# Performance work log

Measured on AMD Instinct MI355X. Metric: run time of the kernel, lower is better.

## Reference

```python
import jax, jax.numpy as jnp
import numpy as np

B, FIN, V, X, Y, Z = 2, 32, 768, 8, 8, 8
K, FOUT = 5, 32
NNZ = V * 8  # ~8 neighbors per vertex


def setup_inputs() -> dict:
    key = jax.random.key(0)
    k1, k2, k3, k4, k5 = jax.random.split(key, 5)
    std = np.sqrt(2.0 / (FIN * K)).astype(np.float32)
    return {
        "lap_rows": jax.random.randint(k1, (NNZ,), 0, V, dtype=jnp.int32),
        "lap_cols": jax.random.randint(k2, (NNZ,), 0, V, dtype=jnp.int32),
        "lap_vals": jax.random.normal(k3, (NNZ,), dtype=jnp.float32) * 0.1,
        "x": jax.random.normal(k4, (B, FIN, V, X, Y, Z), dtype=jnp.float32),
        "weight": jax.random.normal(k5, (K, FIN, FOUT), dtype=jnp.float32) * std,
        "bias": jnp.full((FOUT,), 0.01, dtype=jnp.float32),
    }


def reference(lap_rows, lap_cols, lap_vals, x, weight, bias):
    Bb, Fin, Vv, Xx, Yy, Zz = x.shape
    Kk, _, Fout = weight.shape

    def spmm(v):  # sparse [V,V] @ dense [V,D]
        return jax.ops.segment_sum(lap_vals[:, None] * v[lap_cols],
                                   lap_rows, num_segments=Vv)

    # [B,Fin,V,X,Y,Z] -> [V, Fin*B*X*Y*Z]
    x0 = jnp.transpose(x, (2, 1, 0, 3, 4, 5)).reshape(Vv, -1)
    xs = [x0]
    if Kk > 1:
        x1 = spmm(x0)
        xs.append(x1)
        for _ in range(2, Kk):
            x2 = 2.0 * spmm(x1) - x0
            xs.append(x2)
            x0, x1 = x1, x2
    basis = jnp.stack(xs, axis=0)  # [K, V, Fin*B*X*Y*Z]
    basis = basis.reshape(Kk, Vv, Fin, Bb, Xx, Yy, Zz)
    basis = jnp.transpose(basis, (3, 1, 4, 5, 6, 0, 2))  # [B,V,X,Y,Z,K,Fin]
    out = basis.reshape(-1, Kk * Fin) @ weight.reshape(Kk * Fin, Fout)
    out = out.reshape(Bb, Vv, Xx, Yy, Zz, Fout)
    out = jnp.transpose(out, (0, 5, 1, 2, 3, 4))  # [B,Fout,V,X,Y,Z]
    return out + bias[None, :, None, None, None, None]
```

## Files before the change

### kernel.cpp

```cpp
#include <hip/hip_runtime.h>
#include <stdint.h>

#define V      768
#define FINC   32
#define FOUTC  32
#define XYZ    512
#define NB     2
#define ROWP   40
#define MAXDEG 32
#define EROWS  (MAXDEG + 2)

typedef unsigned short u16;
typedef unsigned int   u32;
typedef short bf16x8 __attribute__((ext_vector_type(8)));
typedef float f32x4  __attribute__((ext_vector_type(4)));
typedef float f32x2  __attribute__((ext_vector_type(2)));

__device__ __forceinline__ u16 f2bf(float f) {
  u32 u = __float_as_uint(f);
  u32 r = u + 0x7fffu + ((u >> 16) & 1u);
  return (u16)(r >> 16);
}
__device__ __forceinline__ float bflo(u32 w) { return __uint_as_float(w << 16); }
__device__ __forceinline__ float bfhi(u32 w) { return __uint_as_float(w & 0xffff0000u); }
__device__ __forceinline__ float bfhi_raw(u32 w) { return __uint_as_float(w); }
__device__ __forceinline__ u32 cvtpk_bf16(float lo, float hi) {
  u32 r;
  asm("v_cvt_pk_bf16_f32 %0, %1, %2" : "=v"(r) : "v"(lo), "v"(hi));
  return r;
}

__global__ __launch_bounds__(64) void build_ell(const int* __restrict__ rows,
                                                const int* __restrict__ cols,
                                                const float* __restrict__ vals,
                                                int nnz,
                                                int2* __restrict__ epair,
                                                int* __restrict__ deg) {
  int v = blockIdx.x;
  int lane = threadIdx.x;
  int cnt = 0;
  for (int base = 0; base < nnz; base += 64) {
    int i = base + lane;
    bool m = (i < nnz) && (rows[i] == v);
    unsigned long long mask = __ballot(m);
    if (m) {
      int pos = cnt + __popcll(mask & ((1ull << lane) - 1ull));
      if (pos < MAXDEG)
        epair[v * MAXDEG + pos] = make_int2(cols[i], __float_as_int(vals[i]));
    }
    cnt += __popcll(mask);
  }
  int d = cnt < MAXDEG ? cnt : MAXDEG;
  for (int p = d + lane; p < MAXDEG; p += 64)
    epair[v * MAXDEG + p] = make_int2(0, 0);
  if (lane == 0) deg[v] = d;
}

__global__ __launch_bounds__(V) void sort_rows(const int2* __restrict__ epair,
                                               const int* __restrict__ deg,
                                               int2* __restrict__ ep3,
                                               int* __restrict__ perm,
                                               int* __restrict__ inv_g,
                                               int* __restrict__ wtrip) {
  __shared__ int sdeg[V];
  __shared__ u16 sinv[V];
  int v = threadIdx.x;
  int d = deg[v];
  sdeg[v] = d;
  __syncthreads();
  int r = 0;
  for (int u = 0; u < V; ++u) {
    int du = sdeg[u];
    r += (du > d) || (du == d && u < v);
  }
  const unsigned long long GPK = 0x8495A6B73210ull;
  int w = (int)((GPK >> (4 * (r >> 6))) & 15ull);
  int p = w * 64 + (r & 63);
  perm[p] = v;
  inv_g[v] = p;
  sinv[v] = (u16)p;
  if ((r & 63) == 0) wtrip[w] = d;
  __syncthreads();
  for (int e = 0; e < EROWS; ++e) {
    int2 o = make_int2(0, 0);
    if (e < d) {
      int2 pe = epair[v * MAXDEG + e];
      o = make_int2((int)sinv[pe.x] * (ROWP * 2), pe.y);
    }
    ep3[e * V + p] = o;
  }
}

__global__ __launch_bounds__(512) void transpose_x(const float* __restrict__ x,
                                                   const int* __restrict__ inv_g,
                                                   u16* __restrict__ xT) {
  int g = blockIdx.x;
  int b = g / V, v = g - b * V;
  int pv = inv_g[v];
  int t = threadIdx.x;
  float vals[FINC];
  const float* src = x + ((size_t)(b * FINC) * V + v) * XYZ + t;
#pragma unroll
  for (int f = 0; f < FINC; ++f) vals[f] = src[(size_t)f * V * XYZ];
  u32 pw[16];
#pragma unroll
  for (int p = 0; p < 16; ++p)
    pw[p] = (u32)f2bf(vals[2 * p]) | ((u32)f2bf(vals[2 * p + 1]) << 16);
  uint4* dst = (uint4*)(xT + ((size_t)(b * XYZ + t) * V + pv) * FINC);
#pragma unroll
  for (int q = 0; q < 4; ++q)
    dst[q] = make_uint4(pw[4 * q], pw[4 * q + 1], pw[4 * q + 2], pw[4 * q + 3]);
}

__global__ __launch_bounds__(1024, 4) void cheb_main(
    const u16* __restrict__ xT, const int2* __restrict__ ep3,
    const int* __restrict__ perm, const int* __restrict__ wtrip,
    const float* __restrict__ weight, const float* __restrict__ bias,
    u32* __restrict__ stage) {
  __shared__ __align__(16) u16   CUR[V * ROWP];
  __shared__ __align__(16) uint4 WF[5][2][64];
  __shared__ u16 PRM[V];
  __shared__ int WT[12];

  int g = blockIdx.x;
  int xcd = g & 7;
  int u = g >> 3;
  int phase = u >> 5;
  int xyz = xcd * 32 + (u & 31) + (phase & 1) * 256;
  int b = phase >> 1;
  int slice = b * XYZ + xyz;

  int tid = threadIdx.x;
  int lane = tid & 63;
  int w = tid >> 6;
  int l15 = lane & 15, l4 = lane >> 4;
  bool gath = tid < V;

  if (tid < 640) {
    int k = tid >> 7, n = (tid >> 6) & 1, ln = tid & 63;
    int a15 = ln & 15, a4 = ln >> 4;
    u32 pw[4];
#pragma unroll
    for (int p = 0; p < 4; ++p) {
      float w0 = weight[(size_t)(k * FINC + a4 * 8 + 2 * p) * FOUTC + n * 16 + a15];
      float w1 = weight[(size_t)(k * FINC + a4 * 8 + 2 * p + 1) * FOUTC + n * 16 + a15];
      pw[p] = (u32)f2bf(w0) | ((u32)f2bf(w1) << 16);
    }
    WF[k][n][ln] = make_uint4(pw[0], pw[1], pw[2], pw[3]);
  }
  if (tid < 12) WT[tid] = wtrip[tid];
  if (gath) PRM[tid] = (u16)perm[tid];
  float bsv[2] = {bias[l15], bias[16 + l15]};

  u32 curpk[16], prevpk[16];
  if (gath) {
    const uint4* src = (const uint4*)(xT + (size_t)slice * V * FINC) + tid * 4;
    uint4* dst = (uint4*)(CUR + tid * ROWP);
#pragma unroll
    for (int j = 0; j < 4; ++j) {
      uint4 q = src[j];
      dst[j] = q;
      curpk[4 * j] = q.x; curpk[4 * j + 1] = q.y;
      curpk[4 * j + 2] = q.z; curpk[4 * j + 3] = q.w;
    }
  }
  __syncthreads();

  int trip = 0;
  if (w < 12) trip = __builtin_amdgcn_readfirstlane(WT[w]);
  const int2* pp = ep3 + tid;

  f32x4 acc[3][2];
#pragma unroll
  for (int a = 0; a < 3; ++a)
#pragma unroll
    for (int n = 0; n < 2; ++n) acc[a][n] = (f32x4){0.f, 0.f, 0.f, 0.f};

  auto gemm_acc = [&](int k) {
    bf16x8 bn0 = *(const bf16x8*)&WF[k][0][lane];
    bf16x8 bn1 = *(const bf16x8*)&WF[k][1][lane];
#pragma unroll
    for (int a = 0; a < 3; ++a) {
      int row = w * 48 + a * 16 + l15;
      bf16x8 af = *(const bf16x8*)(CUR + row * ROWP + l4 * 8);
      acc[a][0] = __builtin_amdgcn_mfma_f32_16x16x32_bf16(af, bn0, acc[a][0], 0, 0, 0);
      acc[a][1] = __builtin_amdgcn_mfma_f32_16x16x32_bf16(af, bn1, acc[a][1], 0, 0, 0);
    }
  };

  f32x2 fa2[16];
  auto gather = [&]() {
#pragma unroll
    for (int j = 0; j < 16; ++j) fa2[j] = (f32x2){0.f, 0.f};
    int2 pe0 = pp[0];
    int2 pe1 = pp[V];
    for (int e = 0; e < trip; ++e) {
      int2 nx = pp[(e + 2) * V];
      float fv = __int_as_float(pe0.y);
      f32x2 fv2 = {fv, fv};
      const uint4* sp = (const uint4*)((const char*)CUR + (u32)pe0.x);
      uint4 qa = sp[0], qb = sp[1], qc = sp[2], qd = sp[3];
      u32 wq[16] = {qa.x, qa.y, qa.z, qa.w, qb.x, qb.y, qb.z, qb.w,
                    qc.x, qc.y, qc.z, qc.w, qd.x, qd.y, qd.z, qd.w};
#pragma unroll
      for (int p = 0; p < 16; ++p) {
        f32x2 s = {bflo(wq[p]), bfhi_raw(wq[p])};
        fa2[p] += fv2 * s;
      }
      pe0 = pe1; pe1 = nx;
    }
  };

  auto store_cur = [&]() {
    uint4* dp = (uint4*)(CUR + tid * ROWP);
#pragma unroll
    for (int j = 0; j < 4; ++j)
      dp[j] = make_uint4(curpk[4 * j], curpk[4 * j + 1], curpk[4 * j + 2], curpk[4 * j + 3]);
  };

  gemm_acc(0);
  if (gath) gather();
  __syncthreads();
  if (gath) {
#pragma unroll
    for (int j = 0; j < 16; ++j) {
      prevpk[j] = curpk[j];
      curpk[j] = cvtpk_bf16(fa2[j][0], fa2[j][1]);
    }
    store_cur();
  }
  __syncthreads();

#pragma unroll
  for (int ph = 1; ph <= 3; ++ph) {
    gemm_acc(ph);
    if (gath) gather();
    __syncthreads();
    if (gath) {
#pragma unroll
      for (int j = 0; j < 16; ++j) {
        u32 pv = prevpk[j];
        float t0 = 2.f * fa2[j][0] - bflo(pv);
        float t1 = 2.f * fa2[j][1] - bfhi(pv);
        prevpk[j] = curpk[j];
        curpk[j] = cvtpk_bf16(t0, t1);
      }
      store_cur();
    }
    __syncthreads();
  }

  gemm_acc(4);

  u32* stg = stage + (size_t)slice * (V * 16);
#pragma unroll
  for (int a = 0; a < 3; ++a) {
#pragma unroll
    for (int r = 0; r < 4; ++r) {
      int vr = PRM[w * 48 + a * 16 + l4 * 4 + r];
      u32 pk = cvtpk_bf16(acc[a][0][r] + bsv[0], acc[a][1][r] + bsv[1]);
      stg[vr * 16 + l15] = pk;
    }
  }
}

#define TO_VT  12
#define TO_PAD 193
__global__ __launch_bounds__(512) void transpose_out(const u32* __restrict__ stage,
                                                     float* __restrict__ out) {
  __shared__ u32 T[64 * TO_PAD];
  int g = blockIdx.x;
  int b = g >> 9, vt = (g >> 3) & 63, xt = g & 7;
  int v0 = vt * TO_VT;
  int xyz0 = xt * 64;
  int t = threadIdx.x;
  const u32* base = stage + (size_t)(b * XYZ + xyz0) * (V * 16) + v0 * 16;
#pragma unroll
  for (int i = 0; i < 6; ++i) {
    int idx4 = i * 512 + t;
    int j = idx4 / 48;
    int c4 = idx4 - j * 48;
    uint4 q = *(const uint4*)(base + (size_t)j * (V * 16) + c4 * 4);
    int w0 = c4 * 4;
    T[j * TO_PAD + w0]     = q.x;
    T[j * TO_PAD + w0 + 1] = q.y;
    T[j * TO_PAD + w0 + 2] = q.z;
    T[j * TO_PAD + w0 + 3] = q.w;
  }
  __syncthreads();
  int wv = t >> 6, lane = t & 63;
#pragma unroll
  for (int i = 0; i < 48; ++i) {
    int fout = wv * 4 + i / 12;
    int vv = i % 12;
    u32 pk = T[lane * TO_PAD + vv * 16 + (fout & 15)];
    float val = (fout < 16) ? bflo(pk) : bfhi(pk);
    out[((size_t)(b * FOUTC + fout) * V + v0 + vv) * XYZ + xyz0 + lane] = val;
  }
}

extern "C" void kernel_launch(void* const* d_in, const int* in_sizes, int n_in,
                              void* d_out, int out_size, void* d_ws, size_t ws_size,
                              hipStream_t stream) {
  const int*   lap_rows = (const int*)d_in[0];
  const int*   lap_cols = (const int*)d_in[1];
  const float* lap_vals = (const float*)d_in[2];
  const float* x        = (const float*)d_in[3];
  const float* weight   = (const float*)d_in[4];
  const float* bias     = (const float*)d_in[5];
  float* out = (float*)d_out;
  int nnz = in_sizes[0];

  char* ws = (char*)d_ws;
  const size_t XT_BYTES = (size_t)NB * XYZ * V * FINC * sizeof(u16);
  const size_t EP_BYTES = (size_t)V * MAXDEG * 8;
  const size_t E3_BYTES = (size_t)EROWS * V * 8;
  u16*  xT    = (u16*)ws;
  u32*  stg   = (u32*)ws;
  int2* epair = (int2*)(ws + XT_BYTES);
  int2* ep3   = (int2*)(ws + XT_BYTES + EP_BYTES);
  int*  deg   = (int*)(ws + XT_BYTES + EP_BYTES + E3_BYTES);
  int*  perm  = (int*)(ws + XT_BYTES + EP_BYTES + E3_BYTES + 3072);
  int*  inv_g = (int*)(ws + XT_BYTES + EP_BYTES + E3_BYTES + 6144);
  int*  wtrip = (int*)(ws + XT_BYTES + EP_BYTES + E3_BYTES + 9216);

  hipLaunchKernelGGL(build_ell, dim3(V), dim3(64), 0, stream,
                     lap_rows, lap_cols, lap_vals, nnz, epair, deg);
  hipLaunchKernelGGL(sort_rows, dim3(1), dim3(V), 0, stream,
                     epair, deg, ep3, perm, inv_g, wtrip);
  hipLaunchKernelGGL(transpose_x, dim3(NB * V), dim3(512), 0, stream, x, inv_g, xT);
  hipLaunchKernelGGL(cheb_main, dim3(NB * XYZ), dim3(1024), 0, stream,
                     xT, ep3, perm, wtrip, weight, bias, stg);
  hipLaunchKernelGGL(transpose_out, dim3(NB * 64 * 8), dim3(512), 0, stream,
                     stg, out);
}
```

Measured before the change: 221.7 us.

## Reorder per-row neighbor lists to spread LDS banks and skip padded edges

The sort kernel now greedily reorders each row's neighbor list so that, at each edge step, lanes in a wave tend to read CUR rows that fall in different LDS bank groups. The intent is to reduce bank conflicts in the gather. The main kernel also loads each row's true degree and skips the LDS reads and FMAs for padded edges past that degree, cutting wasted work for lanes with short rows. The cost is extra serial work in the single-block sort kernel, a new degree array, and a per-iteration branch that can diverge within a wave.

```diff
diff --git a/kernel.cpp b/kernel.cpp
--- a/kernel.cpp
+++ b/kernel.cpp
@@ -61,7 +61,8 @@
                                                int2* __restrict__ ep3,
                                                int* __restrict__ perm,
                                                int* __restrict__ inv_g,
-                                               int* __restrict__ wtrip) {
+                                               int* __restrict__ wtrip,
+                                               int* __restrict__ degp) {
   __shared__ int sdeg[V];
   __shared__ u16 sinv[V];
   int v = threadIdx.x;
@@ -79,13 +80,30 @@
   perm[p] = v;
   inv_g[v] = p;
   sinv[v] = (u16)p;
+  degp[p] = d;
   if ((r & 63) == 0) wtrip[w] = d;
   __syncthreads();
+  int l = p & 63;
+  int nc[MAXDEG]; int nv[MAXDEG];
+  for (int e = 0; e < d; ++e) {
+    int2 pe = epair[v * MAXDEG + e];
+    nc[e] = (int)sinv[pe.x];
+    nv[e] = pe.y;
+  }
+  unsigned used = 0;
   for (int e = 0; e < EROWS; ++e) {
     int2 o = make_int2(0, 0);
     if (e < d) {
-      int2 pe = epair[v * MAXDEG + e];
-      o = make_int2((int)sinv[pe.x] * (ROWP * 2), pe.y);
+      int t = (l + e) & 7;
+      int best = 0, bestd = 9;
+      for (int i = 0; i < d; ++i) {
+        if (used & (1u << i)) continue;
+        int s = (5 * nc[i]) & 7;
+        int dist = (s - t) & 7; if (dist > 4) dist = 8 - dist;
+        if (dist < bestd) { bestd = dist; best = i; if (dist == 0) break; }
+      }
+      used |= 1u << best;
+      o = make_int2(nc[best] * (ROWP * 2), nv[best]);
     }
     ep3[e * V + p] = o;
   }
@@ -115,6 +133,7 @@
 __global__ __launch_bounds__(1024, 4) void cheb_main(
     const u16* __restrict__ xT, const int2* __restrict__ ep3,
     const int* __restrict__ perm, const int* __restrict__ wtrip,
+    const int* __restrict__ degp,
     const float* __restrict__ weight, const float* __restrict__ bias,
     u32* __restrict__ stage) {
   __shared__ __align__(16) u16   CUR[V * ROWP];
@@ -151,6 +170,7 @@
   if (tid < 12) WT[tid] = wtrip[tid];
   if (gath) PRM[tid] = (u16)perm[tid];
   float bsv[2] = {bias[l15], bias[16 + l15]};
+  int myDeg = gath ? degp[tid] : 0;
 
   u32 curpk[16], prevpk[16];
   if (gath) {
@@ -196,16 +216,18 @@
     int2 pe1 = pp[V];
     for (int e = 0; e < trip; ++e) {
       int2 nx = pp[(e + 2) * V];
-      float fv = __int_as_float(pe0.y);
-      f32x2 fv2 = {fv, fv};
-      const uint4* sp = (const uint4*)((const char*)CUR + (u32)pe0.x);
-      uint4 qa = sp[0], qb = sp[1], qc = sp[2], qd = sp[3];
-      u32 wq[16] = {qa.x, qa.y, qa.z, qa.w, qb.x, qb.y, qb.z, qb.w,
-                    qc.x, qc.y, qc.z, qc.w, qd.x, qd.y, qd.z, qd.w};
-#pragma unroll
-      for (int p = 0; p < 16; ++p) {
-        f32x2 s = {bflo(wq[p]), bfhi_raw(wq[p])};
-        fa2[p] += fv2 * s;
+      if (e < myDeg) {
+        float fv = __int_as_float(pe0.y);
+        f32x2 fv2 = {fv, fv};
+        const uint4* sp = (const uint4*)((const char*)CUR + (u32)pe0.x);
+        uint4 qa = sp[0], qb = sp[1], qc = sp[2], qd = sp[3];
+        u32 wq[16] = {qa.x, qa.y, qa.z, qa.w, qb.x, qb.y, qb.z, qb.w,
+                      qc.x, qc.y, qc.z, qc.w, qd.x, qd.y, qd.z, qd.w};
+#pragma unroll
+        for (int p = 0; p < 16; ++p) {
+          f32x2 s = {bflo(wq[p]), bfhi_raw(wq[p])};
+          fa2[p] += fv2 * s;
+        }
       }
       pe0 = pe1; pe1 = nx;
     }
@@ -323,14 +345,15 @@
   int*  perm  = (int*)(ws + XT_BYTES + EP_BYTES + E3_BYTES + 3072);
   int*  inv_g = (int*)(ws + XT_BYTES + EP_BYTES + E3_BYTES + 6144);
   int*  wtrip = (int*)(ws + XT_BYTES + EP_BYTES + E3_BYTES + 9216);
+  int*  degp  = (int*)(ws + XT_BYTES + EP_BYTES + E3_BYTES + 12288);
 
   hipLaunchKernelGGL(build_ell, dim3(V), dim3(64), 0, stream,
                      lap_rows, lap_cols, lap_vals, nnz, epair, deg);
   hipLaunchKernelGGL(sort_rows, dim3(1), dim3(V), 0, stream,
-                     epair, deg, ep3, perm, inv_g, wtrip);
+                     epair, deg, ep3, perm, inv_g, wtrip, degp);
   hipLaunchKernelGGL(transpose_x, dim3(NB * V), dim3(512), 0, stream, x, inv_g, xT);
   hipLaunchKernelGGL(cheb_main, dim3(NB * XYZ), dim3(1024), 0, stream,
-                     xT, ep3, perm, wtrip, weight, bias, stg);
+                     xT, ep3, perm, wtrip, degp, weight, bias, stg);
   hipLaunchKernelGGL(transpose_out, dim3(NB * 64 * 8), dim3(512), 0, stream,
                      stg, out);
 }
```

Result: slower. 284.5 us (+28.3%).
